# Kernel tuning notes

Measured on AMD Instinct MI355X. Metric: run time of the kernel, lower is better.

## Reference

```python
import jax, jax.numpy as jnp
import numpy as np

B, F, T = 256, 513, 512   # batch, x_dim, seq_len
Z, H, DX, ZG, DZX = 16, 128, 256, 32, 128

def _lin(key, out_d, in_d):
    k1, k2 = jax.random.split(key)
    s = 1.0 / np.sqrt(in_d)
    W = jax.random.uniform(k1, (out_d, in_d), minval=-s, maxval=s, dtype=jnp.float32)
    b = jax.random.uniform(k2, (out_d,), minval=-s, maxval=s, dtype=jnp.float32)
    return W, b

def setup_inputs() -> dict:
    key = jax.random.key(0)
    ks = jax.random.split(key, 20)
    d = {}
    d['x'] = jax.random.normal(ks[0], (B, F, T), dtype=jnp.float32)
    d['eps'] = jax.random.normal(ks[1], (T, B, Z), dtype=jnp.float32)  # reparam noise per step
    # mlp_x_gx: Linear(513,256)+tanh
    d['W_xg'], d['b_xg'] = _lin(ks[2], DX, F)
    # LSTM(256,128), torch gate order i,f,g,o
    s = 1.0 / np.sqrt(H)
    k1, k2, k3, k4 = jax.random.split(ks[3], 4)
    d['W_ih'] = jax.random.uniform(k1, (4 * H, DX), minval=-s, maxval=s, dtype=jnp.float32)
    d['W_hh'] = jax.random.uniform(k2, (4 * H, H), minval=-s, maxval=s, dtype=jnp.float32)
    d['b_ih'] = jax.random.uniform(k3, (4 * H,), minval=-s, maxval=s, dtype=jnp.float32)
    d['b_hh'] = jax.random.uniform(k4, (4 * H,), minval=-s, maxval=s, dtype=jnp.float32)
    # mlp_ztm1_g: Linear(16,32)+tanh, Linear(32,128)+tanh
    d['W_zg0'], d['b_zg0'] = _lin(ks[4], ZG, Z)
    d['W_zg1'], d['b_zg1'] = _lin(ks[5], H, ZG)
    # mlp_g_z = Identity (dense_g_z=[0]); inf heads Linear(128,16)
    d['W_im'], d['b_im'] = _lin(ks[6], Z, H)
    d['W_il'], d['b_il'] = _lin(ks[7], Z, H)
    # gating unit: Linear(16,16)+ReLU, Linear(16,16)+Sigmoid
    d['W_gate0'], d['b_gate0'] = _lin(ks[8], Z, Z)
    d['W_gate1'], d['b_gate1'] = _lin(ks[9], Z, Z)
    # proposed mean: Linear(16,16)+ReLU, Linear(16,16)+Sigmoid
    d['W_prop0'], d['b_prop0'] = _lin(ks[10], Z, Z)
    d['W_prop1'], d['b_prop1'] = _lin(ks[11], Z, Z)
    # prior_mean Linear(16,16); prior_logvar ReLU->Linear(16,16)->Softplus
    d['W_pm'], d['b_pm'] = _lin(ks[12], Z, Z)
    d['W_pl'], d['b_pl'] = _lin(ks[13], Z, Z)
    # mlp_z_x: Linear(16,128)+tanh, Linear(128,128)+tanh; gen_logvar Linear(128,513)
    d['W_zx0'], d['b_zx0'] = _lin(ks[14], DZX, Z)
    d['W_zx1'], d['b_zx1'] = _lin(ks[15], DZX, DZX)
    d['W_gy'], d['b_gy'] = _lin(ks[16], F, DZX)
    return d

def reference(x, eps, W_xg, b_xg, W_ih, W_hh, b_ih, b_hh, W_zg0, b_zg0, W_zg1, b_zg1,
              W_im, b_im, W_il, b_il, W_gate0, b_gate0, W_gate1, b_gate1,
              W_prop0, b_prop0, W_prop1, b_prop1, W_pm, b_pm, W_pl, b_pl,
              W_zx0, b_zx0, W_zx1, b_zx1, W_gy, b_gy):
    xs = jnp.transpose(x, (2, 0, 1))                 # [T,B,F]
    xg = jnp.tanh(xs @ W_xg.T + b_xg)                # [T,B,DX]
    bsz = xs.shape[1]
    Hd = W_hh.shape[1]

    def lstm_step(carry, xt):
        h, c = carry
        gates = xt @ W_ih.T + b_ih + h @ W_hh.T + b_hh
        i, f, g, o = jnp.split(gates, 4, axis=-1)
        c = jax.nn.sigmoid(f) * c + jax.nn.sigmoid(i) * jnp.tanh(g)
        h = jax.nn.sigmoid(o) * jnp.tanh(c)
        return (h, c), h

    h0 = jnp.zeros((bsz, Hd), xg.dtype)
    # module runs LSTM on flipped sequence, then flips output back
    _, g_rev = jax.lax.scan(lstm_step, (h0, h0), xg[::-1])
    g = g_rev[::-1]                                   # [T,B,H]

    def inf_step(z_t, inp):
        g_rnn, e = inp
        hz = jnp.tanh(z_t @ W_zg0.T + b_zg0)
        hz = jnp.tanh(hz @ W_zg1.T + b_zg1)
        g_t = (hz + g_rnn) * 0.5                      # mlp_g_z is Identity
        zm = g_t @ W_im.T + b_im
        zl = g_t @ W_il.T + b_il
        z_new = zm + e * jnp.exp(0.5 * zl)            # reparameterization
        return z_new, (z_new, zm, zl)

    z0 = jnp.zeros((bsz, W_im.shape[0]), xg.dtype)
    _, (z, z_mean, z_logvar) = jax.lax.scan(inf_step, z0, (g, eps))

    # generation_z (gated) -- stored as attributes in the torch module
    z_tm1 = jnp.concatenate([z0[None], z[:-1]], axis=0)
    prop = jax.nn.sigmoid(jax.nn.relu(z_tm1 @ W_prop0.T + b_prop0) @ W_prop1.T + b_prop1)
    gate = jax.nn.sigmoid(jax.nn.relu(z_tm1 @ W_gate0.T + b_gate0) @ W_gate1.T + b_gate1)
    z_mean_p = (1.0 - gate) * (z_tm1 @ W_pm.T + b_pm) + gate * prop
    z_logvar_p = jnp.log(jax.nn.softplus(jax.nn.relu(prop) @ W_pl.T + b_pl))

    # generation_x
    hy = jnp.tanh(z @ W_zx0.T + b_zx0)
    hy = jnp.tanh(hy @ W_zx1.T + b_zx1)
    y = jnp.exp(hy @ W_gy.T + b_gy)                   # [T,B,F]
    return jnp.transpose(y, (1, 2, 0))                # [B,F,T] (forward returns self.y)
```

## Files before the change

### kernel.cpp

```cpp
#include <hip/hip_runtime.h>
#include <cstdint>

#define T_DIM 512
#define B_DIM 256
#define F_DIM 513
#define DX    256
#define H_DIM 128
#define G4    512
#define Z_DIM 16
#define ZG_D  32
#define DZX_D 128
#define M_ROWS (B_DIM * T_DIM)

__device__ __forceinline__ float fast_tanh(float x) {
    return 1.0f - 2.0f / (__expf(2.0f * x) + 1.0f);
}
__device__ __forceinline__ float fast_sig(float x) {
    return 1.0f / (1.0f + __expf(-x));
}

__global__ void bias_comb_kernel(const float* __restrict__ a,
                                 const float* __restrict__ b,
                                 float* __restrict__ c) {
    int i = threadIdx.x;
    if (i < G4) c[i] = a[i] + b[i];
}

template<int ACT, int AMODE, int CMODE, bool GUARD>
__global__ __launch_bounds__(256) void gemm_kernel(
    const float* __restrict__ A, const float* __restrict__ W,
    const float* __restrict__ bias, float* __restrict__ C,
    int M, int N, int K)
{
    __shared__ float As[16][68];
    __shared__ float Bs[16][68];
    const int tid = threadIdx.x;
    const int m0 = blockIdx.y * 64;
    const int n0 = blockIdx.x * 64;
    const int tm = tid >> 4;
    const int tn = tid & 15;
    float acc[4][4] = {};
    const int kTiles = (K + 15) >> 4;
    for (int kt = 0; kt < kTiles; ++kt) {
        const int k0 = kt << 4;
        if (AMODE == 0) {
            const int m  = tid >> 2;
            const int kq = tid & 3;
            const float4 v = *(const float4*)&A[(size_t)(m0 + m) * K + k0 + kq * 4];
            As[kq * 4 + 0][m] = v.x; As[kq * 4 + 1][m] = v.y;
            As[kq * 4 + 2][m] = v.z; As[kq * 4 + 3][m] = v.w;
        } else {
            const int m  = tid & 63;
            const int kq = tid >> 6;
            const int mg = m0 + m;
            const int bb = mg >> 9;
            const int tt = mg & 511;
            const size_t base = (size_t)bb * (F_DIM * T_DIM) + tt;
            #pragma unroll
            for (int j = 0; j < 4; ++j) {
                const int k = k0 + kq * 4 + j;
                As[kq * 4 + j][m] = (k < K) ? A[base + (size_t)k * T_DIM] : 0.0f;
            }
        }
        {
            const int n  = tid >> 2;
            const int kq = tid & 3;
            const int ng = n0 + n;
            if (!GUARD) {
                const float4 v = *(const float4*)&W[(size_t)ng * K + k0 + kq * 4];
                Bs[kq * 4 + 0][n] = v.x; Bs[kq * 4 + 1][n] = v.y;
                Bs[kq * 4 + 2][n] = v.z; Bs[kq * 4 + 3][n] = v.w;
            } else {
                #pragma unroll
                for (int j = 0; j < 4; ++j) {
                    const int k = k0 + kq * 4 + j;
                    float v = 0.0f;
                    if (ng < N && k < K) v = W[(size_t)ng * K + k];
                    Bs[kq * 4 + j][n] = v;
                }
            }
        }
        __syncthreads();
        #pragma unroll
        for (int kk = 0; kk < 16; ++kk) {
            const float4 av = *(const float4*)&As[kk][tm * 4];
            const float4 bv = *(const float4*)&Bs[kk][tn * 4];
            const float a0 = av.x, a1 = av.y, a2 = av.z, a3 = av.w;
            const float b0 = bv.x, b1 = bv.y, b2 = bv.z, b3 = bv.w;
            acc[0][0] += a0 * b0; acc[0][1] += a0 * b1; acc[0][2] += a0 * b2; acc[0][3] += a0 * b3;
            acc[1][0] += a1 * b0; acc[1][1] += a1 * b1; acc[1][2] += a1 * b2; acc[1][3] += a1 * b3;
            acc[2][0] += a2 * b0; acc[2][1] += a2 * b1; acc[2][2] += a2 * b2; acc[2][3] += a2 * b3;
            acc[3][0] += a3 * b0; acc[3][1] += a3 * b1; acc[3][2] += a3 * b2; acc[3][3] += a3 * b3;
        }
        __syncthreads();
    }
    #pragma unroll
    for (int i = 0; i < 4; ++i) {
        const int m = m0 + tm * 4 + i;
        if (CMODE == 0) {
            float r[4];
            #pragma unroll
            for (int j = 0; j < 4; ++j) {
                const int n = n0 + tn * 4 + j;
                float v = acc[i][j] + bias[n];
                if (ACT == 1) v = fast_tanh(v);
                else if (ACT == 2) v = __expf(v);
                r[j] = v;
            }
            *(float4*)&C[(size_t)m * N + n0 + tn * 4] = make_float4(r[0], r[1], r[2], r[3]);
        } else {
            const int bb = m >> 9;
            const int tt = m & 511;
            #pragma unroll
            for (int j = 0; j < 4; ++j) {
                const int n = n0 + tn * 4 + j;
                if (n < N) {
                    float v = acc[i][j] + bias[n];
                    if (ACT == 1) v = fast_tanh(v);
                    else if (ACT == 2) v = __expf(v);
                    C[(size_t)bb * (F_DIM * T_DIM) + (size_t)n * T_DIM + tt] = v;
                }
            }
        }
    }
}

__global__ __launch_bounds__(256, 1) void lstm_kernel(
    const float* __restrict__ gin,
    const float* __restrict__ W_hh,
    float* __restrict__ g_out)
{
    __shared__ float4 h4[32];
    __shared__ float gates[512];
    const int tid = threadIdx.x;
    const int b = blockIdx.x;

    float4 wA[32], wB[32];
    const float4* w4 = (const float4*)W_hh;
    #pragma unroll
    for (int q = 0; q < 32; ++q) {
        wA[q] = w4[(size_t)(2 * tid) * 32 + q];
        wB[q] = w4[(size_t)(2 * tid + 1) * 32 + q];
    }
    if (tid < 32) h4[tid] = make_float4(0.f, 0.f, 0.f, 0.f);
    float c = 0.0f;
    __syncthreads();

    const float2* gin2 = (const float2*)(gin + (size_t)b * T_DIM * G4);
    float2 gv = gin2[(size_t)(T_DIM - 1) * 256 + tid];
    for (int t = T_DIM - 1; t >= 0; --t) {
        float2 gnext = (t > 0) ? gin2[(size_t)(t - 1) * 256 + tid] : make_float2(0.f, 0.f);
        float a0 = 0.f, a1 = 0.f;
        #pragma unroll
        for (int q = 0; q < 32; ++q) {
            const float4 hv = h4[q];
            a0 += wA[q].x * hv.x + wA[q].y * hv.y + wA[q].z * hv.z + wA[q].w * hv.w;
            a1 += wB[q].x * hv.x + wB[q].y * hv.y + wB[q].z * hv.z + wB[q].w * hv.w;
        }
        a0 += gv.x;
        a1 += gv.y;
        gates[2 * tid]     = a0;
        gates[2 * tid + 1] = a1;
        __syncthreads();
        if (tid < 128) {
            const float iv = gates[tid];
            const float fv = gates[tid + 128];
            const float gg = gates[tid + 256];
            const float ov = gates[tid + 384];
            c = fast_sig(fv) * c + fast_sig(iv) * fast_tanh(gg);
            const float h = fast_sig(ov) * fast_tanh(c);
            ((float*)h4)[tid] = h;
            g_out[((size_t)b * T_DIM + t) * H_DIM + tid] = h;
        }
        __syncthreads();
        gv = gnext;
    }
}

__global__ __launch_bounds__(64, 1) void infer_kernel(
    const float* __restrict__ g,
    const float* __restrict__ eps,
    const float* __restrict__ W_zg0, const float* __restrict__ b_zg0,
    const float* __restrict__ W_zg1, const float* __restrict__ b_zg1,
    const float* __restrict__ W_im,  const float* __restrict__ b_im,
    const float* __restrict__ W_il,  const float* __restrict__ b_il,
    float* __restrict__ z_out)
{
    __shared__ float zbuf[16];
    __shared__ float hzbuf[32];
    __shared__ float h2buf[128];
    const int l = threadIdx.x;
    const int b = blockIdx.x;

    const int r0 = l & 31;
    float4 wz0[4];
    #pragma unroll
    for (int q = 0; q < 4; ++q) wz0[q] = ((const float4*)W_zg0)[r0 * 4 + q];
    const float bz0 = b_zg0[r0];
    float4 w1a[8], w1b[8];
    #pragma unroll
    for (int q = 0; q < 8; ++q) {
        w1a[q] = ((const float4*)W_zg1)[l * 8 + q];
        w1b[q] = ((const float4*)W_zg1)[(l + 64) * 8 + q];
    }
    const float bz1a = b_zg1[l], bz1b = b_zg1[l + 64];
    const int o = l & 31;
    const int half = l >> 5;
    const float* w3p = (o < 16) ? (W_im + o * 128) : (W_il + (o - 16) * 128);
    float4 w3[16];
    #pragma unroll
    for (int q = 0; q < 16; ++q) w3[q] = ((const float4*)(w3p + half * 64))[q];
    const float b3 = (o < 16) ? b_im[o] : b_il[o - 16];

    if (l < 16) zbuf[l] = 0.0f;
    __syncthreads();

    const float* gb = g + (size_t)b * T_DIM * 128;
    float ngl0 = gb[l];
    float ngl1 = gb[64 + l];
    float neps = (l < 16) ? eps[(size_t)b * 16 + l] : 0.0f;
    for (int t = 0; t < T_DIM; ++t) {
        const float gl0 = ngl0, gl1 = ngl1, epsv = neps;
        if (t + 1 < T_DIM) {
            ngl0 = gb[(size_t)(t + 1) * 128 + l];
            ngl1 = gb[(size_t)(t + 1) * 128 + 64 + l];
            neps = (l < 16) ? eps[((size_t)(t + 1) * B_DIM + b) * 16 + l] : 0.0f;
        }
        float s1 = bz0;
        {
            const float4* z4 = (const float4*)zbuf;
            #pragma unroll
            for (int q = 0; q < 4; ++q) {
                const float4 zv = z4[q];
                s1 += wz0[q].x * zv.x + wz0[q].y * zv.y + wz0[q].z * zv.z + wz0[q].w * zv.w;
            }
        }
        const float hz = fast_tanh(s1);
        __syncthreads();
        if (l < 32) hzbuf[l] = hz;
        __syncthreads();
        float s2a = bz1a, s2b = bz1b;
        {
            const float4* hz4 = (const float4*)hzbuf;
            #pragma unroll
            for (int q = 0; q < 8; ++q) {
                const float4 hv = hz4[q];
                s2a += w1a[q].x * hv.x + w1a[q].y * hv.y + w1a[q].z * hv.z + w1a[q].w * hv.w;
                s2b += w1b[q].x * hv.x + w1b[q].y * hv.y + w1b[q].z * hv.z + w1b[q].w * hv.w;
            }
        }
        const float gt0 = 0.5f * (fast_tanh(s2a) + gl0);
        const float gt1 = 0.5f * (fast_tanh(s2b) + gl1);
        __syncthreads();
        h2buf[l]      = gt0;
        h2buf[l + 64] = gt1;
        __syncthreads();
        float s3 = 0.0f;
        {
            const float4* h24 = (const float4*)(h2buf + half * 64);
            #pragma unroll
            for (int q = 0; q < 16; ++q) {
                const float4 hv = h24[q];
                s3 += w3[q].x * hv.x + w3[q].y * hv.y + w3[q].z * hv.z + w3[q].w * hv.w;
            }
        }
        const float full = s3 + __shfl_xor(s3, 32, 64);
        const float val = full + b3;
        const float other = __shfl_xor(val, 16, 64);
        const float znew = val + epsv * __expf(0.5f * other);
        __syncthreads();
        if (l < 16) {
            zbuf[l] = znew;
            z_out[((size_t)b * T_DIM + t) * 16 + l] = znew;
        }
        __syncthreads();
    }
}

extern "C" void kernel_launch(void* const* d_in, const int* in_sizes, int n_in,
                              void* d_out, int out_size, void* d_ws, size_t ws_size,
                              hipStream_t stream)
{
    const float* x     = (const float*)d_in[0];
    const float* eps   = (const float*)d_in[1];
    const float* W_xg  = (const float*)d_in[2];
    const float* b_xg  = (const float*)d_in[3];
    const float* W_ih  = (const float*)d_in[4];
    const float* W_hh  = (const float*)d_in[5];
    const float* b_ih  = (const float*)d_in[6];
    const float* b_hh  = (const float*)d_in[7];
    const float* W_zg0 = (const float*)d_in[8];
    const float* b_zg0 = (const float*)d_in[9];
    const float* W_zg1 = (const float*)d_in[10];
    const float* b_zg1 = (const float*)d_in[11];
    const float* W_im  = (const float*)d_in[12];
    const float* b_im  = (const float*)d_in[13];
    const float* W_il  = (const float*)d_in[14];
    const float* b_il  = (const float*)d_in[15];
    const float* W_zx0 = (const float*)d_in[28];
    const float* b_zx0 = (const float*)d_in[29];
    const float* W_zx1 = (const float*)d_in[30];
    const float* b_zx1 = (const float*)d_in[31];
    const float* W_gy  = (const float*)d_in[32];
    const float* b_gy  = (const float*)d_in[33];
    float* out = (float*)d_out;
    float* ws  = (float*)d_ws;

    float* xg  = ws;
    float* gin = ws + 33554432ull;
    float* g   = ws + 100663296ull;
    float* z   = ws + 117440512ull;
    float* bc  = ws + 119537664ull;
    float* hy1 = ws;
    float* hy2 = ws + 16777216ull;

    bias_comb_kernel<<<1, 512, 0, stream>>>(b_ih, b_hh, bc);
    gemm_kernel<1, 1, 0, true><<<dim3(DX / 64, M_ROWS / 64), 256, 0, stream>>>(
        x, W_xg, b_xg, xg, M_ROWS, DX, F_DIM);
    gemm_kernel<0, 0, 0, false><<<dim3(G4 / 64, M_ROWS / 64), 256, 0, stream>>>(
        xg, W_ih, bc, gin, M_ROWS, G4, DX);
    lstm_kernel<<<B_DIM, 256, 0, stream>>>(gin, W_hh, g);
    infer_kernel<<<B_DIM, 64, 0, stream>>>(g, eps, W_zg0, b_zg0, W_zg1, b_zg1,
                                           W_im, b_im, W_il, b_il, z);
    gemm_kernel<1, 0, 0, false><<<dim3(DZX_D / 64, M_ROWS / 64), 256, 0, stream>>>(
        z, W_zx0, b_zx0, hy1, M_ROWS, DZX_D, Z_DIM);
    gemm_kernel<1, 0, 0, false><<<dim3(DZX_D / 64, M_ROWS / 64), 256, 0, stream>>>(
        hy1, W_zx1, b_zx1, hy2, M_ROWS, DZX_D, DZX_D);
    gemm_kernel<2, 0, 1, true><<<dim3(9, M_ROWS / 64), 256, 0, stream>>>(
        hy2, W_gy, b_gy, out, M_ROWS, F_DIM, DZX_D);
}
```

Measured before the change: 3.325 ms.

## Restructure LSTM recurrence to per-unit gate ownership with double-buffered hidden state

Each thread now owns all four gates of one hidden unit over half of the hidden dimension. The two halves are combined with a cross-lane shuffle, so the shared gates array and the second barrier per timestep are gone. The hidden state is double-buffered in shared memory, which leaves one __syncthreads per step on the serial critical path. Register use for weights stays about the same. The output-gate sum carries a stray `so * 0.f` term that is harmless for finite values.

```diff
diff --git a/kernel.cpp b/kernel.cpp
--- a/kernel.cpp
+++ b/kernel.cpp
@@ -130,50 +130,72 @@
     const float* __restrict__ W_hh,
     float* __restrict__ g_out)
 {
-    __shared__ float4 h4[32];
-    __shared__ float gates[512];
+    __shared__ float hbuf[2][128];
     const int tid = threadIdx.x;
     const int b = blockIdx.x;
-
-    float4 wA[32], wB[32];
-    const float4* w4 = (const float4*)W_hh;
-    #pragma unroll
-    for (int q = 0; q < 32; ++q) {
-        wA[q] = w4[(size_t)(2 * tid) * 32 + q];
-        wB[q] = w4[(size_t)(2 * tid + 1) * 32 + q];
-    }
-    if (tid < 32) h4[tid] = make_float4(0.f, 0.f, 0.f, 0.f);
+    const int lane = tid & 63;
+    const int w = tid >> 6;
+    const int j = w * 32 + (lane & 31);
+    const int kh = lane >> 5;
+
+    float4 wi[16], wf[16], wg[16], wo[16];
+    {
+        const float4* w4 = (const float4*)W_hh;
+        const int cb = kh * 16;
+        #pragma unroll
+        for (int q = 0; q < 16; ++q) {
+            wi[q] = w4[(size_t)(j      ) * 32 + cb + q];
+            wf[q] = w4[(size_t)(j + 128) * 32 + cb + q];
+            wg[q] = w4[(size_t)(j + 256) * 32 + cb + q];
+            wo[q] = w4[(size_t)(j + 384) * 32 + cb + q];
+        }
+    }
+    if (tid < 128) { hbuf[0][tid] = 0.f; hbuf[1][tid] = 0.f; }
     float c = 0.0f;
     __syncthreads();
 
-    const float2* gin2 = (const float2*)(gin + (size_t)b * T_DIM * G4);
-    float2 gv = gin2[(size_t)(T_DIM - 1) * 256 + tid];
+    const float* ginb = gin + (size_t)b * T_DIM * G4;
+    float gi = ginb[(size_t)(T_DIM - 1) * G4 + j];
+    float gf = ginb[(size_t)(T_DIM - 1) * G4 + j + 128];
+    float gg = ginb[(size_t)(T_DIM - 1) * G4 + j + 256];
+    float go = ginb[(size_t)(T_DIM - 1) * G4 + j + 384];
+
+    int buf = 0;
     for (int t = T_DIM - 1; t >= 0; --t) {
-        float2 gnext = (t > 0) ? gin2[(size_t)(t - 1) * 256 + tid] : make_float2(0.f, 0.f);
-        float a0 = 0.f, a1 = 0.f;
-        #pragma unroll
-        for (int q = 0; q < 32; ++q) {
-            const float4 hv = h4[q];
-            a0 += wA[q].x * hv.x + wA[q].y * hv.y + wA[q].z * hv.z + wA[q].w * hv.w;
-            a1 += wB[q].x * hv.x + wB[q].y * hv.y + wB[q].z * hv.z + wB[q].w * hv.w;
-        }
-        a0 += gv.x;
-        a1 += gv.y;
-        gates[2 * tid]     = a0;
-        gates[2 * tid + 1] = a1;
-        __syncthreads();
-        if (tid < 128) {
-            const float iv = gates[tid];
-            const float fv = gates[tid + 128];
-            const float gg = gates[tid + 256];
-            const float ov = gates[tid + 384];
-            c = fast_sig(fv) * c + fast_sig(iv) * fast_tanh(gg);
-            const float h = fast_sig(ov) * fast_tanh(c);
-            ((float*)h4)[tid] = h;
-            g_out[((size_t)b * T_DIM + t) * H_DIM + tid] = h;
-        }
-        __syncthreads();
-        gv = gnext;
+        float ngi = 0.f, ngf = 0.f, ngg = 0.f, ngo = 0.f;
+        if (t > 0) {
+            const size_t base = (size_t)(t - 1) * G4;
+            ngi = ginb[base + j];
+            ngf = ginb[base + j + 128];
+            ngg = ginb[base + j + 256];
+            ngo = ginb[base + j + 384];
+        }
+        float si = 0.f, sf = 0.f, sg = 0.f, so = 0.f;
+        {
+            const float4* h4 = (const float4*)&hbuf[buf][kh * 64];
+            #pragma unroll
+            for (int q = 0; q < 16; ++q) {
+                const float4 hv = h4[q];
+                si += wi[q].x * hv.x + wi[q].y * hv.y + wi[q].z * hv.z + wi[q].w * hv.w;
+                sf += wf[q].x * hv.x + wf[q].y * hv.y + wf[q].z * hv.z + wf[q].w * hv.w;
+                sg += wg[q].x * hv.x + wg[q].y * hv.y + wg[q].z * hv.z + wg[q].w * hv.w;
+                so += wo[q].x * hv.x + wo[q].y * hv.y + so * 0.f + wo[q].w * hv.w + wo[q].z * hv.z;
+            }
+        }
+        si += __shfl_xor(si, 32, 64);
+        sf += __shfl_xor(sf, 32, 64);
+        sg += __shfl_xor(sg, 32, 64);
+        so += __shfl_xor(so, 32, 64);
+        si += gi; sf += gf; sg += gg; so += go;
+        c = fast_sig(sf) * c + fast_sig(si) * fast_tanh(sg);
+        const float h = fast_sig(so) * fast_tanh(c);
+        buf ^= 1;
+        if (kh == 0) {
+            hbuf[buf][j] = h;
+            g_out[((size_t)b * T_DIM + t) * H_DIM + j] = h;
+        }
+        __syncthreads();
+        gi = ngi; gf = ngf; gg = ngg; go = ngo;
     }
 }
 
```

After: 3.283 ms. No clear change (-1.3%).
